# Performance work log

Hardware: AMD Instinct MI355X
Metric: run time of the kernel (lower is better)

## Reference

```python
import jax, jax.numpy as jnp
import numpy as np

B = 65536

def setup_inputs() -> dict:
    key = jax.random.key(0)
    ks = jax.random.split(key, 6)
    inp = {
        "x": jax.random.normal(ks[0], (B, 784), dtype=jnp.float32),
        "w_conv": jnp.ones((3, 3), dtype=jnp.float32),
        "w1": jax.random.normal(ks[1], (128, 676), dtype=jnp.float32) * 0.04,
        "b1": jnp.zeros((128,), dtype=jnp.float32),
        "w2": jax.random.normal(ks[2], (512, 128), dtype=jnp.float32) * 0.09,
        "b2": jnp.zeros((512,), dtype=jnp.float32),
        "w3": jax.random.normal(ks[3], (256, 512), dtype=jnp.float32) * 0.04,
        "b3": jnp.zeros((256,), dtype=jnp.float32),
        "w4": jax.random.normal(ks[4], (10, 256), dtype=jnp.float32) * 0.06,
        "b4": jnp.zeros((10,), dtype=jnp.float32),
    }
    return inp


def reference(x, w_conv, w1, b1, w2, b2, w3, b3, w4, b4):
    # x: [B, 784] -> [B, 1, 28, 28]; valid 3x3 conv -> [B, 1, 26, 26]
    img = x.reshape(-1, 1, 28, 28)
    kern = w_conv.reshape(1, 1, 3, 3)
    conv = jax.lax.conv_general_dilated(
        img, kern, window_strides=(1, 1), padding="VALID",
        dimension_numbers=("NCHW", "OIHW", "NCHW"))
    # Original detaches conv weights AND wraps output in torch.tensor(...),
    # which cuts the autograd graph at the conv output.
    h = jax.lax.stop_gradient(conv.reshape(conv.shape[0], -1))  # [B, 676]
    h = jax.nn.relu(h @ w1.T + b1)   # [B, 128]
    h = jax.nn.relu(h @ w2.T + b2)   # [B, 512]
    h = jax.nn.relu(h @ w3.T + b3)   # [B, 256]
    return h @ w4.T + b4             # [B, 10]
```

## Files before the change

kernel.cpp:

```cpp
#include <hip/hip_runtime.h>
#include <stdint.h>

typedef _Float16 half8 __attribute__((ext_vector_type(8)));
typedef float    f32x4 __attribute__((ext_vector_type(4)));

static __device__ __forceinline__ void async_cp16(const void* g, void* l) {
  __builtin_amdgcn_global_load_lds(
      (const __attribute__((address_space(1))) uint32_t*)g,
      (__attribute__((address_space(3))) uint32_t*)l,
      16, 0, 0);
}

__global__ void pack_all(const float* __restrict__ w1, const float* __restrict__ wc,
                         const float* __restrict__ w2, const float* __restrict__ w3,
                         const float* __restrict__ w4,
                         _Float16* __restrict__ pw1, _Float16* __restrict__ pw2,
                         _Float16* __restrict__ pw3, _Float16* __restrict__ pw4)
{
  int idx = (int)blockIdx.x * 256 + (int)threadIdx.x;

  if (idx < 114688) {
    const int e = idx & 7, lane = (idx >> 3) & 63, f = idx >> 9;
    const int nt = f & 7, gks = f >> 3;
    const int n = nt * 16 + (lane & 15);
    const int k = gks * 32 + ((lane >> 4) << 3) + e;
    float val = 0.0f;
    if (k < 784) {
      const int pr = k / 28, pc = k % 28;
      #pragma unroll
      for (int i = 0; i < 3; ++i)
        #pragma unroll
        for (int j = 0; j < 3; ++j) {
          const int orow = pr - i, ocol = pc - j;
          if (orow >= 0 && orow < 26 && ocol >= 0 && ocol < 26)
            val += wc[i * 3 + j] * w1[n * 676 + orow * 26 + ocol];
        }
    }
    pw1[idx] = (_Float16)val;
    return;
  }
  idx -= 114688;
  if (idx < 65536) {
    const int e = idx & 7, lane = (idx >> 3) & 63, f = idx >> 9;
    const int nt = f & 7, ks = (f >> 3) & 3, g = f >> 5;
    const int n = g * 128 + nt * 16 + (lane & 15);
    const int k = ks * 32 + ((lane >> 4) << 3) + e;
    pw2[idx] = (_Float16)w2[n * 128 + k];
    return;
  }
  idx -= 65536;
  if (idx < 131072) {
    const int e = idx & 7, lane = (idx >> 3) & 63, f = idx >> 9;
    const int nt = f & 7, ks = (f >> 3) & 3, c = f >> 5;
    const int n = ((c & 1) * 8 + nt) * 16 + (lane & 15);
    const int k = ((c >> 1) * 4 + ks) * 32 + ((lane >> 4) << 3) + e;
    pw3[idx] = (_Float16)w3[n * 512 + k];
    return;
  }
  idx -= 131072;
  if (idx < 4096) {
    const int e = idx & 7, lane = (idx >> 3) & 63, f = idx >> 9;
    const int n = lane & 15;
    const int k = f * 32 + ((lane >> 4) << 3) + e;
    pw4[idx] = (_Float16)((n < 10) ? w4[n * 256 + k] : 0.0f);
    return;
  }
}

__global__ __launch_bounds__(512, 2)
void fused_mlp(const float* __restrict__ x,
               const _Float16* __restrict__ pw1, const _Float16* __restrict__ pw2,
               const _Float16* __restrict__ pw3, const _Float16* __restrict__ pw4,
               const float* __restrict__ b1, const float* __restrict__ b2,
               const float* __restrict__ b3, const float* __restrict__ b4,
               float* __restrict__ out)
{
  __shared__ char wbuf[2][32768];
  __shared__ char tbuf[8][8192];

  const int tid  = (int)threadIdx.x;
  const int lane = tid & 63;
  const int wid  = tid >> 6;
  const int ln   = lane & 15;
  const int hi   = lane >> 4;
  const int rowBase = (int)blockIdx.x * 128 + wid * 16;
  char* tb = tbuf[wid];

  auto stage = [&](int p) {
    const char* src; int nb;
    if (p < 7)       { src = (const char*)pw1 + (size_t)p * 32768; nb = 32768; }
    else if (p < 19) {
      const int j = p - 7, g = j / 3, r = j - g * 3;
      if (r == 0)      src = (const char*)pw2 + (size_t)g * 32768;
      else if (r == 1) src = (const char*)pw3 + (size_t)(2 * g) * 32768;
      else             src = (const char*)pw3 + (size_t)(2 * g + 1) * 32768;
      nb = 32768;
    } else           { src = (const char*)pw4; nb = 8192; }
    char* dst = wbuf[p & 1];
    const int rounds = nb >> 13;
    for (int r = 0; r < rounds; ++r)
      async_cp16(src + r * 8192 + tid * 16, dst + r * 8192 + wid * 1024);
  };

  auto Bfrag = [&](const char* buf, int f) -> half8 {
    return *(const half8*)(buf + (((f << 6) + lane) << 4));
  };
  auto twrite = [&](int row, int col, float v) {
    const int off = (row << 9) + ((col << 1) ^ ((row & 7) << 4));
    *(_Float16*)(tb + off) = (_Float16)v;
  };
  auto tread = [&](int ks) -> half8 {
    const int off = (ln << 9) + (((ks << 6) + (hi << 4)) ^ ((ln & 7) << 4));
    return *(const half8*)(tb + off);
  };

  const float* xrow = x + (size_t)(rowBase + ln) * 784;
  auto loadA = [&](int gks) -> half8 {
    half8 h;
    const int k0 = gks * 32 + hi * 8;
    if (k0 < 784) {
      const f32x4 v0 = *(const f32x4*)(xrow + k0);
      const f32x4 v1 = *(const f32x4*)(xrow + k0 + 4);
      #pragma unroll
      for (int e = 0; e < 4; ++e) { h[e] = (_Float16)v0[e]; h[4 + e] = (_Float16)v1[e]; }
    } else {
      #pragma unroll
      for (int e = 0; e < 8; ++e) h[e] = (_Float16)0.0f;
    }
    return h;
  };

  f32x4 acc1[8], acc3[16];
  #pragma unroll
  for (int nt = 0; nt < 8; ++nt) {
    const float bv = b1[nt * 16 + ln];
    f32x4 a = {bv, bv, bv, bv}; acc1[nt] = a;
  }
  #pragma unroll
  for (int q = 0; q < 16; ++q) {
    const float bv = b3[q * 16 + ln];
    f32x4 a = {bv, bv, bv, bv}; acc3[q] = a;
  }

  stage(0);
  __syncthreads();

  #pragma unroll
  for (int kc = 0; kc < 7; ++kc) {
    stage(kc + 1);
    const char* bw = wbuf[kc & 1];
    half8 a[4];
    #pragma unroll
    for (int ks = 0; ks < 4; ++ks) a[ks] = loadA(kc * 4 + ks);
    #pragma unroll
    for (int ks = 0; ks < 4; ++ks)
      #pragma unroll
      for (int nt = 0; nt < 8; ++nt)
        acc1[nt] = __builtin_amdgcn_mfma_f32_16x16x32_f16(
            a[ks], Bfrag(bw, ks * 8 + nt), acc1[nt], 0, 0, 0);
    __syncthreads();
  }

  half8 a1h[4];
  #pragma unroll
  for (int nt = 0; nt < 8; ++nt)
    #pragma unroll
    for (int r = 0; r < 4; ++r)
      twrite(hi * 4 + r, nt * 16 + ln, fmaxf(acc1[nt][r], 0.0f));
  #pragma unroll
  for (int ks = 0; ks < 4; ++ks) a1h[ks] = tread(ks);

  #pragma unroll
  for (int g = 0; g < 4; ++g) {
    const int p = 7 + 3 * g;
    half8 a2c[4];

    stage(p + 1);
    {
      const char* bw = wbuf[p & 1];
      f32x4 acc2[8];
      #pragma unroll
      for (int nt = 0; nt < 8; ++nt) {
        const float bv = b2[g * 128 + nt * 16 + ln];
        f32x4 a = {bv, bv, bv, bv}; acc2[nt] = a;
      }
      #pragma unroll
      for (int ks = 0; ks < 4; ++ks)
        #pragma unroll
        for (int nt = 0; nt < 8; ++nt)
          acc2[nt] = __builtin_amdgcn_mfma_f32_16x16x32_f16(
              a1h[ks], Bfrag(bw, ks * 8 + nt), acc2[nt], 0, 0, 0);
      #pragma unroll
      for (int nt = 0; nt < 8; ++nt)
        #pragma unroll
        for (int r = 0; r < 4; ++r)
          twrite(hi * 4 + r, nt * 16 + ln, fmaxf(acc2[nt][r], 0.0f));
      #pragma unroll
      for (int ks = 0; ks < 4; ++ks) a2c[ks] = tread(ks);
    }
    __syncthreads();

    stage(p + 2);
    {
      const char* bw = wbuf[(p + 1) & 1];
      #pragma unroll
      for (int ks = 0; ks < 4; ++ks)
        #pragma unroll
        for (int nt = 0; nt < 8; ++nt)
          acc3[nt] = __builtin_amdgcn_mfma_f32_16x16x32_f16(
              a2c[ks], Bfrag(bw, ks * 8 + nt), acc3[nt], 0, 0, 0);
    }
    __syncthreads();

    stage(p + 3);
    {
      const char* bw = wbuf[p & 1];
      #pragma unroll
      for (int ks = 0; ks < 4; ++ks)
        #pragma unroll
        for (int nt = 0; nt < 8; ++nt)
          acc3[8 + nt] = __builtin_amdgcn_mfma_f32_16x16x32_f16(
              a2c[ks], Bfrag(bw, ks * 8 + nt), acc3[8 + nt], 0, 0, 0);
    }
    __syncthreads();
  }

  {
    #pragma unroll
    for (int q = 0; q < 16; ++q)
      #pragma unroll
      for (int r = 0; r < 4; ++r)
        twrite(hi * 4 + r, q * 16 + ln, fmaxf(acc3[q][r], 0.0f));
    half8 a3h[8];
    #pragma unroll
    for (int ks = 0; ks < 8; ++ks) a3h[ks] = tread(ks);

    const float bv = (ln < 10) ? b4[ln] : 0.0f;
    f32x4 acc4 = {bv, bv, bv, bv};
    const char* bw = wbuf[1];
    #pragma unroll
    for (int ks = 0; ks < 8; ++ks)
      acc4 = __builtin_amdgcn_mfma_f32_16x16x32_f16(
          a3h[ks], Bfrag(bw, ks), acc4, 0, 0, 0);

    if (ln < 10) {
      #pragma unroll
      for (int r = 0; r < 4; ++r)
        out[(size_t)(rowBase + hi * 4 + r) * 10 + ln] = acc4[r];
    }
  }
}


extern "C" void kernel_launch(void* const* d_in, const int* in_sizes, int n_in,
                              void* d_out, int out_size, void* d_ws, size_t ws_size,
                              hipStream_t stream)
{
  const float* x     = (const float*)d_in[0];
  const float* wconv = (const float*)d_in[1];
  const float* w1    = (const float*)d_in[2];
  const float* b1    = (const float*)d_in[3];
  const float* w2    = (const float*)d_in[4];
  const float* b2    = (const float*)d_in[5];
  const float* w3    = (const float*)d_in[6];
  const float* b3    = (const float*)d_in[7];
  const float* w4    = (const float*)d_in[8];
  const float* b4    = (const float*)d_in[9];
  float* out = (float*)d_out;
  char*  ws  = (char*)d_ws;

  _Float16* pw1 = (_Float16*)(ws + 0);
  _Float16* pw2 = (_Float16*)(ws + 229376);
  _Float16* pw3 = (_Float16*)(ws + 360448);
  _Float16* pw4 = (_Float16*)(ws + 622592);

  pack_all<<<1232, 256, 0, stream>>>(w1, wconv, w2, w3, w4, pw1, pw2, pw3, pw4);
  fused_mlp<<<512, 512, 0, stream>>>(x, pw1, pw2, pw3, pw4, b1, b2, b3, b4, out);
}
```

Baseline: 340.8 us.

## Halve LDS staging buffers to fit four blocks per CU, prefetch x ahead

Cuts the weight staging buffers from 32KB to 16KB and the per-wave transpose tile from 8KB to 4KB, so the kernel uses half the LDS. It raises launch bounds to 4 blocks per CU. The weight pipeline becomes twice as many half-size stages, and the layer-3 output transpose is done in two halves. The x tiles are now loaded one stage ahead, overlapping the global loads with MFMA. In exchange there are twice as many barriers, and a tighter register budget (acc3 has 64 floats) may cause spills.

```diff
diff --git a/kernel.cpp b/kernel.cpp
--- a/kernel.cpp
+++ b/kernel.cpp
@@ -67,7 +67,7 @@
   }
 }
 
-__global__ __launch_bounds__(512, 2)
+__global__ __launch_bounds__(512, 4)
 void fused_mlp(const float* __restrict__ x,
                const _Float16* __restrict__ pw1, const _Float16* __restrict__ pw2,
                const _Float16* __restrict__ pw3, const _Float16* __restrict__ pw4,
@@ -75,8 +75,8 @@
                const float* __restrict__ b3, const float* __restrict__ b4,
                float* __restrict__ out)
 {
-  __shared__ char wbuf[2][32768];
-  __shared__ char tbuf[8][8192];
+  __shared__ char wbuf[2][16384];
+  __shared__ char tbuf[8][4096];
 
   const int tid  = (int)threadIdx.x;
   const int lane = tid & 63;
@@ -87,30 +87,27 @@
   char* tb = tbuf[wid];
 
   auto stage = [&](int p) {
-    const char* src; int nb;
-    if (p < 7)       { src = (const char*)pw1 + (size_t)p * 32768; nb = 32768; }
-    else if (p < 19) {
-      const int j = p - 7, g = j / 3, r = j - g * 3;
-      if (r == 0)      src = (const char*)pw2 + (size_t)g * 32768;
-      else if (r == 1) src = (const char*)pw3 + (size_t)(2 * g) * 32768;
-      else             src = (const char*)pw3 + (size_t)(2 * g + 1) * 32768;
-      nb = 32768;
-    } else           { src = (const char*)pw4; nb = 8192; }
+    const char* src; int rounds = 2;
+    if (p < 14)      src = (const char*)pw1 + (size_t)p * 16384;
+    else if (p < 38) {
+      const int j = p - 14, g = j / 6, r = j - g * 6;
+      src = (r < 2) ? (const char*)pw2 + (size_t)(g * 32768 + r * 16384)
+                    : (const char*)pw3 + (size_t)(g * 65536 + (r - 2) * 16384);
+    } else { src = (const char*)pw4; rounds = 1; }
     char* dst = wbuf[p & 1];
-    const int rounds = nb >> 13;
     for (int r = 0; r < rounds; ++r)
-      async_cp16(src + r * 8192 + tid * 16, dst + r * 8192 + wid * 1024);
+      async_cp16(src + r * 8192 + (size_t)tid * 16, dst + r * 8192 + wid * 1024);
   };
 
   auto Bfrag = [&](const char* buf, int f) -> half8 {
     return *(const half8*)(buf + (((f << 6) + lane) << 4));
   };
   auto twrite = [&](int row, int col, float v) {
-    const int off = (row << 9) + ((col << 1) ^ ((row & 7) << 4));
+    const int off = (row << 8) + ((col << 1) ^ ((row & 7) << 4));
     *(_Float16*)(tb + off) = (_Float16)v;
   };
   auto tread = [&](int ks) -> half8 {
-    const int off = (ln << 9) + (((ks << 6) + (hi << 4)) ^ ((ln & 7) << 4));
+    const int off = (ln << 8) + (((ks << 6) + (hi << 4)) ^ ((ln & 7) << 4));
     return *(const half8*)(tb + off);
   };
 
@@ -130,66 +127,78 @@
     return h;
   };
 
-  f32x4 acc1[8], acc3[16];
+  f32x4 acc1[8];
   #pragma unroll
   for (int nt = 0; nt < 8; ++nt) {
     const float bv = b1[nt * 16 + ln];
     f32x4 a = {bv, bv, bv, bv}; acc1[nt] = a;
   }
+
+  stage(0);
+  half8 ap0 = loadA(0), ap1 = loadA(1);
+  __syncthreads();
+
+  for (int p = 0; p < 14; ++p) {
+    stage(p + 1);
+    const half8 a0 = ap0, a1 = ap1;
+    if (p < 13) { ap0 = loadA(2 * p + 2); ap1 = loadA(2 * p + 3); }
+    const char* bw = wbuf[p & 1];
+    #pragma unroll
+    for (int nt = 0; nt < 8; ++nt)
+      acc1[nt] = __builtin_amdgcn_mfma_f32_16x16x32_f16(a0, Bfrag(bw, nt), acc1[nt], 0, 0, 0);
+    #pragma unroll
+    for (int nt = 0; nt < 8; ++nt)
+      acc1[nt] = __builtin_amdgcn_mfma_f32_16x16x32_f16(a1, Bfrag(bw, 8 + nt), acc1[nt], 0, 0, 0);
+    __syncthreads();
+  }
+
+  half8 a1h[4];
+  #pragma unroll
+  for (int nt = 0; nt < 8; ++nt)
+    #pragma unroll
+    for (int r = 0; r < 4; ++r)
+      twrite(hi * 4 + r, nt * 16 + ln, fmaxf(acc1[nt][r], 0.0f));
+  #pragma unroll
+  for (int ks = 0; ks < 4; ++ks) a1h[ks] = tread(ks);
+
+  f32x4 acc3[16];
   #pragma unroll
   for (int q = 0; q < 16; ++q) {
     const float bv = b3[q * 16 + ln];
     f32x4 a = {bv, bv, bv, bv}; acc3[q] = a;
   }
 
-  stage(0);
-  __syncthreads();
-
-  #pragma unroll
-  for (int kc = 0; kc < 7; ++kc) {
-    stage(kc + 1);
-    const char* bw = wbuf[kc & 1];
-    half8 a[4];
-    #pragma unroll
-    for (int ks = 0; ks < 4; ++ks) a[ks] = loadA(kc * 4 + ks);
-    #pragma unroll
-    for (int ks = 0; ks < 4; ++ks)
-      #pragma unroll
-      for (int nt = 0; nt < 8; ++nt)
-        acc1[nt] = __builtin_amdgcn_mfma_f32_16x16x32_f16(
-            a[ks], Bfrag(bw, ks * 8 + nt), acc1[nt], 0, 0, 0);
-    __syncthreads();
-  }
-
-  half8 a1h[4];
-  #pragma unroll
-  for (int nt = 0; nt < 8; ++nt)
-    #pragma unroll
-    for (int r = 0; r < 4; ++r)
-      twrite(hi * 4 + r, nt * 16 + ln, fmaxf(acc1[nt][r], 0.0f));
-  #pragma unroll
-  for (int ks = 0; ks < 4; ++ks) a1h[ks] = tread(ks);
-
-  #pragma unroll
   for (int g = 0; g < 4; ++g) {
-    const int p = 7 + 3 * g;
+    const int pb = 14 + 6 * g;
     half8 a2c[4];
-
-    stage(p + 1);
-    {
-      const char* bw = wbuf[p & 1];
-      f32x4 acc2[8];
-      #pragma unroll
-      for (int nt = 0; nt < 8; ++nt) {
-        const float bv = b2[g * 128 + nt * 16 + ln];
-        f32x4 a = {bv, bv, bv, bv}; acc2[nt] = a;
-      }
-      #pragma unroll
-      for (int ks = 0; ks < 4; ++ks)
-        #pragma unroll
-        for (int nt = 0; nt < 8; ++nt)
-          acc2[nt] = __builtin_amdgcn_mfma_f32_16x16x32_f16(
-              a1h[ks], Bfrag(bw, ks * 8 + nt), acc2[nt], 0, 0, 0);
+    f32x4 acc2[8];
+    #pragma unroll
+    for (int nt = 0; nt < 8; ++nt) {
+      const float bv = b2[g * 128 + nt * 16 + ln];
+      f32x4 a = {bv, bv, bv, bv}; acc2[nt] = a;
+    }
+
+    stage(pb + 1);
+    {
+      const char* bw = wbuf[0];
+      #pragma unroll
+      for (int nt = 0; nt < 8; ++nt)
+        acc2[nt] = __builtin_amdgcn_mfma_f32_16x16x32_f16(a1h[0], Bfrag(bw, nt), acc2[nt], 0, 0, 0);
+      #pragma unroll
+      for (int nt = 0; nt < 8; ++nt)
+        acc2[nt] = __builtin_amdgcn_mfma_f32_16x16x32_f16(a1h[1], Bfrag(bw, 8 + nt), acc2[nt], 0, 0, 0);
+    }
+    __syncthreads();
+
+    stage(pb + 2);
+    {
+      const char* bw = wbuf[1];
+      #pragma unroll
+      for (int nt = 0; nt < 8; ++nt)
+        acc2[nt] = __builtin_amdgcn_mfma_f32_16x16x32_f16(a1h[2], Bfrag(bw, nt), acc2[nt], 0, 0, 0);
+      #pragma unroll
+      for (int nt = 0; nt < 8; ++nt)
+        acc2[nt] = __builtin_amdgcn_mfma_f32_16x16x32_f16(a1h[3], Bfrag(bw, 8 + nt), acc2[nt], 0, 0, 0);
       #pragma unroll
       for (int nt = 0; nt < 8; ++nt)
         #pragma unroll
@@ -200,48 +209,78 @@
     }
     __syncthreads();
 
-    stage(p + 2);
-    {
-      const char* bw = wbuf[(p + 1) & 1];
-      #pragma unroll
-      for (int ks = 0; ks < 4; ++ks)
-        #pragma unroll
-        for (int nt = 0; nt < 8; ++nt)
-          acc3[nt] = __builtin_amdgcn_mfma_f32_16x16x32_f16(
-              a2c[ks], Bfrag(bw, ks * 8 + nt), acc3[nt], 0, 0, 0);
-    }
-    __syncthreads();
-
-    stage(p + 3);
-    {
-      const char* bw = wbuf[p & 1];
-      #pragma unroll
-      for (int ks = 0; ks < 4; ++ks)
-        #pragma unroll
-        for (int nt = 0; nt < 8; ++nt)
-          acc3[8 + nt] = __builtin_amdgcn_mfma_f32_16x16x32_f16(
-              a2c[ks], Bfrag(bw, ks * 8 + nt), acc3[8 + nt], 0, 0, 0);
+    stage(pb + 3);
+    {
+      const char* bw = wbuf[0];
+      #pragma unroll
+      for (int nt = 0; nt < 8; ++nt)
+        acc3[nt] = __builtin_amdgcn_mfma_f32_16x16x32_f16(a2c[0], Bfrag(bw, nt), acc3[nt], 0, 0, 0);
+      #pragma unroll
+      for (int nt = 0; nt < 8; ++nt)
+        acc3[nt] = __builtin_amdgcn_mfma_f32_16x16x32_f16(a2c[1], Bfrag(bw, 8 + nt), acc3[nt], 0, 0, 0);
+    }
+    __syncthreads();
+
+    stage(pb + 4);
+    {
+      const char* bw = wbuf[1];
+      #pragma unroll
+      for (int nt = 0; nt < 8; ++nt)
+        acc3[nt] = __builtin_amdgcn_mfma_f32_16x16x32_f16(a2c[2], Bfrag(bw, nt), acc3[nt], 0, 0, 0);
+      #pragma unroll
+      for (int nt = 0; nt < 8; ++nt)
+        acc3[nt] = __builtin_amdgcn_mfma_f32_16x16x32_f16(a2c[3], Bfrag(bw, 8 + nt), acc3[nt], 0, 0, 0);
+    }
+    __syncthreads();
+
+    stage(pb + 5);
+    {
+      const char* bw = wbuf[0];
+      #pragma unroll
+      for (int nt = 0; nt < 8; ++nt)
+        acc3[8 + nt] = __builtin_amdgcn_mfma_f32_16x16x32_f16(a2c[0], Bfrag(bw, nt), acc3[8 + nt], 0, 0, 0);
+      #pragma unroll
+      for (int nt = 0; nt < 8; ++nt)
+        acc3[8 + nt] = __builtin_amdgcn_mfma_f32_16x16x32_f16(a2c[1], Bfrag(bw, 8 + nt), acc3[8 + nt], 0, 0, 0);
+    }
+    __syncthreads();
+
+    stage(pb + 6);
+    {
+      const char* bw = wbuf[1];
+      #pragma unroll
+      for (int nt = 0; nt < 8; ++nt)
+        acc3[8 + nt] = __builtin_amdgcn_mfma_f32_16x16x32_f16(a2c[2], Bfrag(bw, nt), acc3[8 + nt], 0, 0, 0);
+      #pragma unroll
+      for (int nt = 0; nt < 8; ++nt)
+        acc3[8 + nt] = __builtin_amdgcn_mfma_f32_16x16x32_f16(a2c[3], Bfrag(bw, 8 + nt), acc3[8 + nt], 0, 0, 0);
     }
     __syncthreads();
   }
 
   {
-    #pragma unroll
-    for (int q = 0; q < 16; ++q)
+    half8 a3h[8];
+    #pragma unroll
+    for (int q = 0; q < 8; ++q)
       #pragma unroll
       for (int r = 0; r < 4; ++r)
         twrite(hi * 4 + r, q * 16 + ln, fmaxf(acc3[q][r], 0.0f));
-    half8 a3h[8];
-    #pragma unroll
-    for (int ks = 0; ks < 8; ++ks) a3h[ks] = tread(ks);
+    #pragma unroll
+    for (int ks = 0; ks < 4; ++ks) a3h[ks] = tread(ks);
+    #pragma unroll
+    for (int q = 0; q < 8; ++q)
+      #pragma unroll
+      for (int r = 0; r < 4; ++r)
+        twrite(hi * 4 + r, q * 16 + ln, fmaxf(acc3[8 + q][r], 0.0f));
+    #pragma unroll
+    for (int ks = 0; ks < 4; ++ks) a3h[4 + ks] = tread(ks);
 
     const float bv = (ln < 10) ? b4[ln] : 0.0f;
     f32x4 acc4 = {bv, bv, bv, bv};
-    const char* bw = wbuf[1];
+    const char* bw = wbuf[0];
     #pragma unroll
     for (int ks = 0; ks < 8; ++ks)
-      acc4 = __builtin_amdgcn_mfma_f32_16x16x32_f16(
-          a3h[ks], Bfrag(bw, ks), acc4, 0, 0, 0);
+      acc4 = __builtin_amdgcn_mfma_f32_16x16x32_f16(a3h[ks], Bfrag(bw, ks), acc4, 0, 0, 0);
 
     if (ln < 10) {
       #pragma unroll
```

After: 415.1 us. 21.8% more time.

## Switch fused MLP to 32x32x16 MFMA with 64-row blocks and N-split waves

Applied to the files above, without the earlier changes.

Rewrites the fused MLP kernel around 32x32x16 MFMA tiles. Each block now handles 64 rows, split into 2 row groups of 32, and the 4 waves in a group split the output columns. The grid doubles to 1024 blocks and the launch bound asks for 4 blocks per CU. Weights are repacked for the new fragment layout, and the K=784 padding to 896 is dropped. The activation of the first layer is prefetched one stage ahead. The goal is to stop every wave reading the full weight fragments, cut LDS traffic per MFMA, and raise occupancy. In exchange it adds more block-wide syncs around a shared transpose buffer, and the last layer must run in two halves.

```diff
diff --git a/kernel.cpp b/kernel.cpp
--- a/kernel.cpp
+++ b/kernel.cpp
@@ -1,8 +1,9 @@
 #include <hip/hip_runtime.h>
 #include <stdint.h>
 
-typedef _Float16 half8 __attribute__((ext_vector_type(8)));
-typedef float    f32x4 __attribute__((ext_vector_type(4)));
+typedef _Float16 half8  __attribute__((ext_vector_type(8)));
+typedef float    f32x4  __attribute__((ext_vector_type(4)));
+typedef float    f32x16 __attribute__((ext_vector_type(16)));
 
 static __device__ __forceinline__ void async_cp16(const void* g, void* l) {
   __builtin_amdgcn_global_load_lds(
@@ -19,13 +20,14 @@
 {
   int idx = (int)blockIdx.x * 256 + (int)threadIdx.x;
 
-  if (idx < 114688) {
-    const int e = idx & 7, lane = (idx >> 3) & 63, f = idx >> 9;
-    const int nt = f & 7, gks = f >> 3;
-    const int n = nt * 16 + (lane & 15);
-    const int k = gks * 32 + ((lane >> 4) << 3) + e;
+  if (idx < 100352) {
+    const int e = idx & 7, lane = (idx >> 3) & 63, t = idx >> 9;
+    const int c = t / 28, fl = t - c * 28;
+    const int ks_in = fl >> 2, nt = fl & 3;
+    const int n = nt * 32 + (lane & 31);
+    const int k = (c * 7 + ks_in) * 16 + ((lane >> 5) << 3) + e;
     float val = 0.0f;
-    if (k < 784) {
+    {
       const int pr = k / 28, pc = k % 28;
       #pragma unroll
       for (int i = 0; i < 3; ++i)
@@ -39,35 +41,37 @@
     pw1[idx] = (_Float16)val;
     return;
   }
-  idx -= 114688;
+  idx -= 100352;
   if (idx < 65536) {
-    const int e = idx & 7, lane = (idx >> 3) & 63, f = idx >> 9;
-    const int nt = f & 7, ks = (f >> 3) & 3, g = f >> 5;
-    const int n = g * 128 + nt * 16 + (lane & 15);
-    const int k = ks * 32 + ((lane >> 4) << 3) + e;
+    const int e = idx & 7, lane = (idx >> 3) & 63, t = idx >> 9;
+    const int g = t >> 5, fl = t & 31;
+    const int ks_in = fl >> 2, nt = fl & 3;
+    const int n = g * 128 + nt * 32 + (lane & 31);
+    const int k = ks_in * 16 + ((lane >> 5) << 3) + e;
     pw2[idx] = (_Float16)w2[n * 128 + k];
     return;
   }
   idx -= 65536;
   if (idx < 131072) {
-    const int e = idx & 7, lane = (idx >> 3) & 63, f = idx >> 9;
-    const int nt = f & 7, ks = (f >> 3) & 3, c = f >> 5;
-    const int n = ((c & 1) * 8 + nt) * 16 + (lane & 15);
-    const int k = ((c >> 1) * 4 + ks) * 32 + ((lane >> 4) << 3) + e;
+    const int e = idx & 7, lane = (idx >> 3) & 63, t = idx >> 9;
+    const int cc = t >> 5, fl = t & 31;
+    const int ks_in = fl >> 3, nt = fl & 7;
+    const int n = nt * 32 + (lane & 31);
+    const int k = (cc * 4 + ks_in) * 16 + ((lane >> 5) << 3) + e;
     pw3[idx] = (_Float16)w3[n * 512 + k];
     return;
   }
   idx -= 131072;
-  if (idx < 4096) {
-    const int e = idx & 7, lane = (idx >> 3) & 63, f = idx >> 9;
-    const int n = lane & 15;
-    const int k = f * 32 + ((lane >> 4) << 3) + e;
+  if (idx < 8192) {
+    const int e = idx & 7, lane = (idx >> 3) & 63, t = idx >> 9;
+    const int n = lane & 31;
+    const int k = t * 16 + ((lane >> 5) << 3) + e;
     pw4[idx] = (_Float16)((n < 10) ? w4[n * 256 + k] : 0.0f);
     return;
   }
 }
 
-__global__ __launch_bounds__(512, 2)
+__global__ __launch_bounds__(512, 4)
 void fused_mlp(const float* __restrict__ x,
                const _Float16* __restrict__ pw1, const _Float16* __restrict__ pw2,
                const _Float16* __restrict__ pw3, const _Float16* __restrict__ pw4,
@@ -76,177 +80,199 @@
                float* __restrict__ out)
 {
   __shared__ char wbuf[2][32768];
-  __shared__ char tbuf[8][8192];
+  __shared__ char tbuf[16384];
 
   const int tid  = (int)threadIdx.x;
   const int lane = tid & 63;
   const int wid  = tid >> 6;
-  const int ln   = lane & 15;
-  const int hi   = lane >> 4;
-  const int rowBase = (int)blockIdx.x * 128 + wid * 16;
-  char* tb = tbuf[wid];
+  const int l31  = lane & 31;
+  const int lh   = lane >> 5;
+  const int rg   = wid >> 2;
+  const int nq   = wid & 3;
+  const int rowBase = (int)blockIdx.x * 64 + rg * 32;
 
   auto stage = [&](int p) {
     const char* src; int nb;
-    if (p < 7)       { src = (const char*)pw1 + (size_t)p * 32768; nb = 32768; }
+    if (p < 7)       { src = (const char*)pw1 + (size_t)p * 28672; nb = 28672; }
     else if (p < 19) {
       const int j = p - 7, g = j / 3, r = j - g * 3;
-      if (r == 0)      src = (const char*)pw2 + (size_t)g * 32768;
-      else if (r == 1) src = (const char*)pw3 + (size_t)(2 * g) * 32768;
-      else             src = (const char*)pw3 + (size_t)(2 * g + 1) * 32768;
-      nb = 32768;
-    } else           { src = (const char*)pw4; nb = 8192; }
+      if (r == 0) { src = (const char*)pw2 + (size_t)g * 32768; nb = 32768; }
+      else        { src = (const char*)pw3 + (size_t)g * 65536 + (size_t)(r - 1) * 32768; nb = 32768; }
+    } else           { src = (const char*)pw4; nb = 16384; }
     char* dst = wbuf[p & 1];
-    const int rounds = nb >> 13;
-    for (int r = 0; r < rounds; ++r)
-      async_cp16(src + r * 8192 + tid * 16, dst + r * 8192 + wid * 1024);
+    for (int off = tid * 16; off < nb; off += 8192)
+      async_cp16(src + off, dst + off);
   };
 
   auto Bfrag = [&](const char* buf, int f) -> half8 {
-    return *(const half8*)(buf + (((f << 6) + lane) << 4));
-  };
-  auto twrite = [&](int row, int col, float v) {
-    const int off = (row << 9) + ((col << 1) ^ ((row & 7) << 4));
-    *(_Float16*)(tb + off) = (_Float16)v;
-  };
-  auto tread = [&](int ks) -> half8 {
-    const int off = (ln << 9) + (((ks << 6) + (hi << 4)) ^ ((ln & 7) << 4));
-    return *(const half8*)(tb + off);
-  };
-
-  const float* xrow = x + (size_t)(rowBase + ln) * 784;
+    return *(const half8*)(buf + (f << 10) + (lane << 4));
+  };
+  auto twr = [&](int r32, int c, float v) {
+    *(_Float16*)(tbuf + ((rg * 32 + r32) << 8) + ((c * 2) ^ ((r32 & 7) << 4))) = (_Float16)v;
+  };
+  auto trd = [&](int ks) -> half8 {
+    const int koff = (ks * 16 + lh * 8) * 2;
+    return *(const half8*)(tbuf + ((rg * 32 + l31) << 8) + (koff ^ ((l31 & 7) << 4)));
+  };
+
+  const float* xrow = x + (size_t)(rowBase + l31) * 784;
   auto loadA = [&](int gks) -> half8 {
+    const int k0 = gks * 16 + lh * 8;
+    const f32x4 v0 = *(const f32x4*)(xrow + k0);
+    const f32x4 v1 = *(const f32x4*)(xrow + k0 + 4);
     half8 h;
-    const int k0 = gks * 32 + hi * 8;
-    if (k0 < 784) {
-      const f32x4 v0 = *(const f32x4*)(xrow + k0);
-      const f32x4 v1 = *(const f32x4*)(xrow + k0 + 4);
-      #pragma unroll
-      for (int e = 0; e < 4; ++e) { h[e] = (_Float16)v0[e]; h[4 + e] = (_Float16)v1[e]; }
-    } else {
-      #pragma unroll
-      for (int e = 0; e < 8; ++e) h[e] = (_Float16)0.0f;
-    }
+    #pragma unroll
+    for (int e = 0; e < 4; ++e) { h[e] = (_Float16)v0[e]; h[4 + e] = (_Float16)v1[e]; }
     return h;
   };
 
-  f32x4 acc1[8], acc3[16];
+  f32x16 acc1;
+  {
+    const float bv = b1[nq * 32 + l31];
+    #pragma unroll
+    for (int r = 0; r < 16; ++r) acc1[r] = bv;
+  }
+
+  stage(0);
+  half8 ap[7];
   #pragma unroll
-  for (int nt = 0; nt < 8; ++nt) {
-    const float bv = b1[nt * 16 + ln];
-    f32x4 a = {bv, bv, bv, bv}; acc1[nt] = a;
-  }
+  for (int i = 0; i < 7; ++i) ap[i] = loadA(i);
+  __syncthreads();
+
   #pragma unroll
-  for (int q = 0; q < 16; ++q) {
-    const float bv = b3[q * 16 + ln];
-    f32x4 a = {bv, bv, bv, bv}; acc3[q] = a;
-  }
-
-  stage(0);
-  __syncthreads();
-
-  #pragma unroll
-  for (int kc = 0; kc < 7; ++kc) {
-    stage(kc + 1);
-    const char* bw = wbuf[kc & 1];
-    half8 a[4];
-    #pragma unroll
-    for (int ks = 0; ks < 4; ++ks) a[ks] = loadA(kc * 4 + ks);
-    #pragma unroll
-    for (int ks = 0; ks < 4; ++ks)
-      #pragma unroll
-      for (int nt = 0; nt < 8; ++nt)
-        acc1[nt] = __builtin_amdgcn_mfma_f32_16x16x32_f16(
-            a[ks], Bfrag(bw, ks * 8 + nt), acc1[nt], 0, 0, 0);
-    __syncthreads();
-  }
-
-  half8 a1h[4];
-  #pragma unroll
-  for (int nt = 0; nt < 8; ++nt)
-    #pragma unroll
-    for (int r = 0; r < 4; ++r)
-      twrite(hi * 4 + r, nt * 16 + ln, fmaxf(acc1[nt][r], 0.0f));
-  #pragma unroll
-  for (int ks = 0; ks < 4; ++ks) a1h[ks] = tread(ks);
+  for (int p = 0; p < 7; ++p) {
+    stage(p + 1);
+    half8 ac[7];
+    #pragma unroll
+    for (int i = 0; i < 7; ++i) ac[i] = ap[i];
+    if (p < 6) {
+      #pragma unroll
+      for (int i = 0; i < 7; ++i) ap[i] = loadA((p + 1) * 7 + i);
+    }
+    const char* bw = wbuf[p & 1];
+    #pragma unroll
+    for (int i = 0; i < 7; ++i)
+      acc1 = __builtin_amdgcn_mfma_f32_32x32x16_f16(ac[i], Bfrag(bw, i * 4 + nq), acc1, 0, 0, 0);
+    if (p == 6) {
+      #pragma unroll
+      for (int r = 0; r < 16; ++r) {
+        const int r32 = (r & 3) + 8 * (r >> 2) + 4 * lh;
+        twr(r32, nq * 32 + l31, fmaxf(acc1[r], 0.0f));
+      }
+    }
+    __syncthreads();
+  }
+
+  half8 a1h[8];
+  f32x16 acc3[2];
+  {
+    const float bva = b3[nq * 64 + l31], bvb = b3[nq * 64 + 32 + l31];
+    #pragma unroll
+    for (int r = 0; r < 16; ++r) { acc3[0][r] = bva; acc3[1][r] = bvb; }
+  }
 
   #pragma unroll
   for (int g = 0; g < 4; ++g) {
     const int p = 7 + 3 * g;
-    half8 a2c[4];
 
     stage(p + 1);
+    if (g == 0) {
+      #pragma unroll
+      for (int ks = 0; ks < 8; ++ks) a1h[ks] = trd(ks);
+    }
+    f32x16 acc2;
+    {
+      const float bv = b2[g * 128 + nq * 32 + l31];
+      #pragma unroll
+      for (int r = 0; r < 16; ++r) acc2[r] = bv;
+    }
     {
       const char* bw = wbuf[p & 1];
-      f32x4 acc2[8];
-      #pragma unroll
-      for (int nt = 0; nt < 8; ++nt) {
-        const float bv = b2[g * 128 + nt * 16 + ln];
-        f32x4 a = {bv, bv, bv, bv}; acc2[nt] = a;
+      #pragma unroll
+      for (int ks = 0; ks < 8; ++ks)
+        acc2 = __builtin_amdgcn_mfma_f32_32x32x16_f16(a1h[ks], Bfrag(bw, ks * 4 + nq), acc2, 0, 0, 0);
+    }
+    __syncthreads();
+    #pragma unroll
+    for (int r = 0; r < 16; ++r) {
+      const int r32 = (r & 3) + 8 * (r >> 2) + 4 * lh;
+      twr(r32, nq * 32 + l31, fmaxf(acc2[r], 0.0f));
+    }
+    __syncthreads();
+
+    {
+      stage(p + 2);
+      half8 a2c[4];
+      #pragma unroll
+      for (int ks = 0; ks < 4; ++ks) a2c[ks] = trd(ks);
+      const char* bw = wbuf[(p + 1) & 1];
+      #pragma unroll
+      for (int ks = 0; ks < 4; ++ks)
+        #pragma unroll
+        for (int t = 0; t < 2; ++t)
+          acc3[t] = __builtin_amdgcn_mfma_f32_32x32x16_f16(
+              a2c[ks], Bfrag(bw, ks * 8 + nq * 2 + t), acc3[t], 0, 0, 0);
+      __syncthreads();
+    }
+    {
+      stage(p + 3);
+      half8 a2c[4];
+      #pragma unroll
+      for (int ks = 0; ks < 4; ++ks) a2c[ks] = trd(4 + ks);
+      const char* bw = wbuf[(p + 2) & 1];
+      #pragma unroll
+      for (int ks = 0; ks < 4; ++ks)
+        #pragma unroll
+        for (int t = 0; t < 2; ++t)
+          acc3[t] = __builtin_amdgcn_mfma_f32_32x32x16_f16(
+              a2c[ks], Bfrag(bw, ks * 8 + nq * 2 + t), acc3[t], 0, 0, 0);
+      __syncthreads();
+    }
+  }
+
+  {
+    const char* bw = wbuf[1];
+    f32x16 acc4;
+    {
+      const float bv = (l31 < 10) ? b4[l31] : 0.0f;
+      #pragma unroll
+      for (int r = 0; r < 16; ++r) acc4[r] = bv;
+    }
+    if (nq < 2) {
+      #pragma unroll
+      for (int t = 0; t < 2; ++t)
+        #pragma unroll
+        for (int r = 0; r < 16; ++r) {
+          const int r32 = (r & 3) + 8 * (r >> 2) + 4 * lh;
+          twr(r32, nq * 64 + t * 32 + l31, fmaxf(acc3[t][r], 0.0f));
+        }
+    }
+    __syncthreads();
+    #pragma unroll
+    for (int ks = 0; ks < 8; ++ks)
+      acc4 = __builtin_amdgcn_mfma_f32_32x32x16_f16(trd(ks), Bfrag(bw, ks), acc4, 0, 0, 0);
+    __syncthreads();
+    if (nq >= 2) {
+      #pragma unroll
+      for (int t = 0; t < 2; ++t)
+        #pragma unroll
+        for (int r = 0; r < 16; ++r) {
+          const int r32 = (r & 3) + 8 * (r >> 2) + 4 * lh;
+          twr(r32, (nq - 2) * 64 + t * 32 + l31, fmaxf(acc3[t][r], 0.0f));
+        }
+    }
+    __syncthreads();
+    #pragma unroll
+    for (int ks = 0; ks < 8; ++ks)
+      acc4 = __builtin_amdgcn_mfma_f32_32x32x16_f16(trd(ks), Bfrag(bw, 8 + ks), acc4, 0, 0, 0);
+
+    if (nq == 0) {
+      #pragma unroll
+      for (int r = 0; r < 16; ++r) {
+        const int r32 = (r & 3) + 8 * (r >> 2) + 4 * lh;
+        if (l31 < 10)
+          out[(size_t)(rowBase + r32) * 10 + l31] = acc4[r];
       }
-      #pragma unroll
-      for (int ks = 0; ks < 4; ++ks)
-        #pragma unroll
-        for (int nt = 0; nt < 8; ++nt)
-          acc2[nt] = __builtin_amdgcn_mfma_f32_16x16x32_f16(
-              a1h[ks], Bfrag(bw, ks * 8 + nt), acc2[nt], 0, 0, 0);
-      #pragma unroll
-      for (int nt = 0; nt < 8; ++nt)
-        #pragma unroll
-        for (int r = 0; r < 4; ++r)
-          twrite(hi * 4 + r, nt * 16 + ln, fmaxf(acc2[nt][r], 0.0f));
-      #pragma unroll
-      for (int ks = 0; ks < 4; ++ks) a2c[ks] = tread(ks);
-    }
-    __syncthreads();
-
-    stage(p + 2);
-    {
-      const char* bw = wbuf[(p + 1) & 1];
-      #pragma unroll
-      for (int ks = 0; ks < 4; ++ks)
-        #pragma unroll
-        for (int nt = 0; nt < 8; ++nt)
-          acc3[nt] = __builtin_amdgcn_mfma_f32_16x16x32_f16(
-              a2c[ks], Bfrag(bw, ks * 8 + nt), acc3[nt], 0, 0, 0);
-    }
-    __syncthreads();
-
-    stage(p + 3);
-    {
-      const char* bw = wbuf[p & 1];
-      #pragma unroll
-      for (int ks = 0; ks < 4; ++ks)
-        #pragma unroll
-        for (int nt = 0; nt < 8; ++nt)
-          acc3[8 + nt] = __builtin_amdgcn_mfma_f32_16x16x32_f16(
-              a2c[ks], Bfrag(bw, ks * 8 + nt), acc3[8 + nt], 0, 0, 0);
-    }
-    __syncthreads();
-  }
-
-  {
-    #pragma unroll
-    for (int q = 0; q < 16; ++q)
-      #pragma unroll
-      for (int r = 0; r < 4; ++r)
-        twrite(hi * 4 + r, q * 16 + ln, fmaxf(acc3[q][r], 0.0f));
-    half8 a3h[8];
-    #pragma unroll
-    for (int ks = 0; ks < 8; ++ks) a3h[ks] = tread(ks);
-
-    const float bv = (ln < 10) ? b4[ln] : 0.0f;
-    f32x4 acc4 = {bv, bv, bv, bv};
-    const char* bw = wbuf[1];
-    #pragma unroll
-    for (int ks = 0; ks < 8; ++ks)
-      acc4 = __builtin_amdgcn_mfma_f32_16x16x32_f16(
-          a3h[ks], Bfrag(bw, ks), acc4, 0, 0, 0);
-
-    if (ln < 10) {
-      #pragma unroll
-      for (int r = 0; r < 4; ++r)
-        out[(size_t)(rowBase + hi * 4 + r) * 10 + ln] = acc4[r];
     }
   }
 }
@@ -270,10 +296,10 @@
   char*  ws  = (char*)d_ws;
 
   _Float16* pw1 = (_Float16*)(ws + 0);
-  _Float16* pw2 = (_Float16*)(ws + 229376);
-  _Float16* pw3 = (_Float16*)(ws + 360448);
-  _Float16* pw4 = (_Float16*)(ws + 622592);
-
-  pack_all<<<1232, 256, 0, stream>>>(w1, wconv, w2, w3, w4, pw1, pw2, pw3, pw4);
-  fused_mlp<<<512, 512, 0, stream>>>(x, pw1, pw2, pw3, pw4, b1, b2, b3, b4, out);
+  _Float16* pw2 = (_Float16*)(ws + 200704);
+  _Float16* pw3 = (_Float16*)(ws + 331776);
+  _Float16* pw4 = (_Float16*)(ws + 593920);
+
+  pack_all<<<1192, 256, 0, stream>>>(w1, wconv, w2, w3, w4, pw1, pw2, pw3, pw4);
+  fused_mlp<<<1024, 512, 0, stream>>>(x, pw1, pw2, pw3, pw4, b1, b2, b3, b4, out);
 }
```

Measured after the change: 364.4 us. 1.07x slower.
